# Kernel tuning notes

Measured on AMD Instinct MI355X. Metric: run time of the kernel, lower is better.

## Reference

```python
import jax, jax.numpy as jnp
import numpy as np
from itertools import combinations

NUM_AUG = 10
EPS = 0.01
GAM3 = 0.01
NUM_PAIRS = 500


def setup_inputs() -> dict:
    key = jax.random.key(0)
    m, p = 4000, 256
    kx, ky = jax.random.split(key)
    X = jax.random.normal(kx, (m, p), dtype=jnp.float32)
    y = jax.random.randint(ky, (m,), 0, 400, dtype=jnp.int64)
    num_imgs = m // NUM_AUG
    # deterministic stand-in for np.random.choice over all image pairs
    rng = np.random.default_rng(0)
    pair_combs = np.array(list(combinations(range(num_imgs), 2)))
    sample_idx = rng.choice(len(pair_combs), NUM_PAIRS)
    sample_pairs = jnp.asarray(pair_combs[sample_idx], dtype=jnp.int32)  # [500, 2]
    return {"X": X, "y": y, "sample_pairs": sample_pairs}


def _pair_logdets(X, sample_pairs):
    # X: [m, p] so W = X.T is [p, m]; diagonal Pi selects num_aug columns of W
    # per image, i.e. contiguous rows of X -> W Pi W^T == seg^T @ seg.
    m, p = X.shape
    aug = jnp.arange(NUM_AUG)
    cols_i = sample_pairs[:, 0:1] * NUM_AUG + aug          # [S, 10]
    cols_j = sample_pairs[:, 1:2] * NUM_AUG + aug          # [S, 10]
    cols_pair = jnp.concatenate([cols_i, cols_j], axis=1)  # [S, 20]
    I = jnp.eye(p, dtype=X.dtype)

    def ld(cols, tr_pi):
        seg = X[cols]                                      # [S, k, p]
        gram = jnp.einsum('skp,skq->spq', seg, seg)        # [S, p, p] = W Pi W^T
        scalar = p / ((tr_pi + 1e-8) * EPS)
        return jnp.linalg.slogdet(I + scalar * gram)[1]    # [S]

    ld_pair = ld(cols_pair, 2.0 * NUM_AUG)  # trace(Pi) = 20
    ld_i = ld(cols_i, 1.0 * NUM_AUG)        # trace(Pi_i) = 10
    ld_j = ld(cols_j, 1.0 * NUM_AUG)        # trace(Pi_j) = 10
    return ld_pair, ld_i, ld_j


def reference(X, y, sample_pairs):
    ld_pair, ld_i, ld_j = _pair_logdets(X, sample_pairs)
    compress_loss_empi_ortho = jnp.mean(ld_pair - 0.5 * ld_i - 0.5 * ld_j)
    discrimn_loss_empi = jnp.mean(ld_pair)            # loss_d / num_pairs
    compress_loss_empi = jnp.mean(ld_i + ld_j)        # loss_c / num_pairs (detached in torch)
    total_loss_empi = GAM3 * -compress_loss_empi_ortho
    return (total_loss_empi, discrimn_loss_empi, compress_loss_empi,
            compress_loss_empi_ortho)
```

## Files before the change

kernel.cpp:

```cpp
#include <hip/hip_runtime.h>
#include <math.h>

#define NUM_AUG 10
#define S_PAIRS 500
#define P 256

typedef __attribute__((ext_vector_type(8))) short bf16x8;
typedef __attribute__((ext_vector_type(16))) float f32x16;

#define C_PAIR ((float)(256.0 / ((20.0 + 1e-8) * 0.01)))
#define C_SING ((float)(256.0 / ((10.0 + 1e-8) * 0.01)))

__device__ __forceinline__ unsigned short f2bf(float f) {
  unsigned u = __float_as_uint(f);
  unsigned r = (u + 0x7fffu + ((u >> 16) & 1u)) >> 16;
  return (unsigned short)r;
}

__global__ __launch_bounds__(64) void pair_kernel(
    const float* __restrict__ X,
    const int* __restrict__ pairs,
    float* __restrict__ out2 ) {
  __shared__ uint4 Sb4[32 * 512 / 16];
  __shared__ float G[20][21];
  char* Sb = (char*)Sb4;

  const int s = blockIdx.x;
  const int lane = threadIdx.x;
  const int i0 = pairs[2 * s + 0] * NUM_AUG;
  const int j0 = pairs[2 * s + 1] * NUM_AUG;

#pragma unroll
  for (int r = 0; r < 20; ++r) {
    const int gr = (r < 10) ? (i0 + r) : (j0 + (r - 10));
    const float4 v = *((const float4*)(X + (size_t)gr * P) + lane);
    uint2 w;
    w.x = (unsigned)f2bf(v.x) | ((unsigned)f2bf(v.y) << 16);
    w.y = (unsigned)f2bf(v.z) | ((unsigned)f2bf(v.w) << 16);
    const int off = r * 512 + ((lane * 8) ^ ((r & 15) << 4));
    *(uint2*)(Sb + off) = w;
  }
  __syncthreads();

  const int row = lane & 31;
  const int kg = lane >> 5;
  f32x16 acc0, acc1;
#pragma unroll
  for (int i = 0; i < 16; ++i) { acc0[i] = 0.f; acc1[i] = 0.f; }
#pragma unroll
  for (int kk = 0; kk < 16; ++kk) {
    const int cb = kk * 32 + kg * 16;
    const bf16x8 f = *(const bf16x8*)(Sb + row * 512 + (cb ^ ((row & 15) << 4)));
    if (kk & 1)
      acc1 = __builtin_amdgcn_mfma_f32_32x32x16_bf16(f, f, acc1, 0, 0, 0);
    else
      acc0 = __builtin_amdgcn_mfma_f32_32x32x16_bf16(f, f, acc0, 0, 0, 0);
  }
#pragma unroll
  for (int rg = 0; rg < 16; ++rg) {
    const int grow = (rg & 3) + 8 * (rg >> 2) + 4 * kg;
    if (grow < 20 && row < 20) G[grow][row] = acc0[rg] + acc1[rg];
  }
  __syncthreads();

  const int grp = (lane < 32) ? 0 : (lane < 48) ? 1 : 2;
  const int base = (grp == 0) ? 0 : (grp == 1) ? 32 : 48;
  const int li = lane - base;
  const int n = (grp == 0) ? 20 : 10;
  const float cf = (grp == 0) ? C_PAIR : C_SING;
  const int r0 = (grp == 2) ? 10 : 0;

  float a[20];
#pragma unroll
  for (int k = 0; k < 20; ++k) {
    float g = 0.f;
    if (li < n && k < n) g = G[r0 + li][r0 + k];
    a[k] = cf * g + ((li == k) ? 1.f : 0.f);
  }

  float ld_acc = 0.f;
#pragma unroll
  for (int j = 0; j < 20; ++j) {
    const float dj = __shfl(a[j], base + j, 64);
    const float Ljj = sqrtf(dj);
    const float inv = 1.0f / Ljj;
    const float Lij = a[j] * inv;
    if (li == j && j < n) ld_acc += logf(Ljj);
#pragma unroll
    for (int k = j + 1; k < 20; ++k) {
      const float ck = __shfl(Lij, base + k, 64);
      if (k < n && li >= k) a[k] = fmaf(-Lij, ck, a[k]);
    }
  }

  float vp = (lane < 32) ? ld_acc : 0.f;
  float vs = (lane >= 32) ? ld_acc : 0.f;
#pragma unroll
  for (int m = 1; m < 64; m <<= 1) {
    vp += __shfl_xor(vp, m, 64);
    vs += __shfl_xor(vs, m, 64);
  }
  if (lane == 0) {
    out2[2 * s + 0] = 2.f * vp;
    out2[2 * s + 1] = 2.f * vs;
  }
}

__global__ __launch_bounds__(64) void reduce_kernel(
    const float* __restrict__ out2, float* __restrict__ out) {
  const int lane = threadIdx.x;
  float sp = 0.f, sij = 0.f;
#pragma unroll
  for (int s = lane; s < S_PAIRS; s += 64) {
    const float2 v = *(const float2*)(out2 + 2 * s);
    sp += v.x;
    sij += v.y;
  }
#pragma unroll
  for (int m = 1; m < 64; m <<= 1) {
    sp += __shfl_xor(sp, m, 64);
    sij += __shfl_xor(sij, m, 64);
  }
  if (lane == 0) {
    const float mp = sp / (float)S_PAIRS;
    const float mij = sij / (float)S_PAIRS;
    const float ortho = mp - 0.5f * mij;
    out[0] = -0.01f * ortho;
    out[1] = mp;
    out[2] = mij;
    out[3] = ortho;
  }
}

extern "C" void kernel_launch(void* const* d_in, const int* in_sizes, int n_in,
                              void* d_out, int out_size, void* d_ws, size_t ws_size,
                              hipStream_t stream) {
  const float* X = (const float*)d_in[0];
  const int* pairs = (const int*)d_in[2];
  float* out = (float*)d_out;
  float* ws = (float*)d_ws;

  pair_kernel<<<S_PAIRS, 64, 0, stream>>>(X, pairs, ws);
  reduce_kernel<<<1, 64, 0, stream>>>(ws, out);
}
```

Before: 16.32 us.

## Fuse final reduction into pair kernel via per-block flags and spin-wait

Replaces the separate reduction kernel launch with a last-block reduction inside the pair kernel. Each block publishes its partial sums with a release store and sets a per-block flag, and block S-1 spins until all flags are set, then reduces. A hipMemsetAsync clears the flags before each launch, so the saved kernel launch is swapped for a memset plus a spin-wait. The design can deadlock if block S-1 gets scheduled before other blocks can run, though with 500 small blocks all of them should fit resident on the device.

```diff
diff --git a/kernel.cpp b/kernel.cpp
--- a/kernel.cpp
+++ b/kernel.cpp
@@ -11,16 +11,20 @@
 #define C_PAIR ((float)(256.0 / ((20.0 + 1e-8) * 0.01)))
 #define C_SING ((float)(256.0 / ((10.0 + 1e-8) * 0.01)))
 
+union pack2f { float f[2]; unsigned long long u; };
+
 __device__ __forceinline__ unsigned short f2bf(float f) {
   unsigned u = __float_as_uint(f);
   unsigned r = (u + 0x7fffu + ((u >> 16) & 1u)) >> 16;
   return (unsigned short)r;
 }
 
-__global__ __launch_bounds__(64) void pair_kernel(
+__global__ __launch_bounds__(64) void fused_kernel(
     const float* __restrict__ X,
     const int* __restrict__ pairs,
-    float* __restrict__ out2 ) {
+    unsigned long long* __restrict__ partial,
+    unsigned* __restrict__ flags,
+    float* __restrict__ out) {
   __shared__ uint4 Sb4[32 * 512 / 16];
   __shared__ float G[20][21];
   char* Sb = (char*)Sb4;
@@ -100,35 +104,47 @@
     vp += __shfl_xor(vp, m, 64);
     vs += __shfl_xor(vs, m, 64);
   }
+
   if (lane == 0) {
-    out2[2 * s + 0] = 2.f * vp;
-    out2[2 * s + 1] = 2.f * vs;
+    pack2f p;
+    p.f[0] = 2.f * vp;
+    p.f[1] = 2.f * vs;
+    __hip_atomic_store(&partial[s], p.u, __ATOMIC_RELEASE, __HIP_MEMORY_SCOPE_AGENT);
+    __hip_atomic_store(&flags[s], 1u, __ATOMIC_RELEASE, __HIP_MEMORY_SCOPE_AGENT);
   }
-}
 
-__global__ __launch_bounds__(64) void reduce_kernel(
-    const float* __restrict__ out2, float* __restrict__ out) {
-  const int lane = threadIdx.x;
-  float sp = 0.f, sij = 0.f;
+  if (s == S_PAIRS - 1) {
+    bool mine;
+    do {
+      mine = true;
 #pragma unroll
-  for (int s = lane; s < S_PAIRS; s += 64) {
-    const float2 v = *(const float2*)(out2 + 2 * s);
-    sp += v.x;
-    sij += v.y;
-  }
+      for (int t = lane; t < S_PAIRS; t += 64)
+        mine = mine &&
+               (__hip_atomic_load(&flags[t], __ATOMIC_ACQUIRE, __HIP_MEMORY_SCOPE_AGENT) != 0u);
+    } while (!__all(mine));
+
+    float sp = 0.f, sij = 0.f;
 #pragma unroll
-  for (int m = 1; m < 64; m <<= 1) {
-    sp += __shfl_xor(sp, m, 64);
-    sij += __shfl_xor(sij, m, 64);
-  }
-  if (lane == 0) {
-    const float mp = sp / (float)S_PAIRS;
-    const float mij = sij / (float)S_PAIRS;
-    const float ortho = mp - 0.5f * mij;
-    out[0] = -0.01f * ortho;
-    out[1] = mp;
-    out[2] = mij;
-    out[3] = ortho;
+    for (int t = lane; t < S_PAIRS; t += 64) {
+      pack2f p;
+      p.u = __hip_atomic_load(&partial[t], __ATOMIC_RELAXED, __HIP_MEMORY_SCOPE_AGENT);
+      sp += p.f[0];
+      sij += p.f[1];
+    }
+#pragma unroll
+    for (int m = 1; m < 64; m <<= 1) {
+      sp += __shfl_xor(sp, m, 64);
+      sij += __shfl_xor(sij, m, 64);
+    }
+    if (lane == 0) {
+      const float mp = sp / (float)S_PAIRS;
+      const float mij = sij / (float)S_PAIRS;
+      const float ortho = mp - 0.5f * mij;
+      out[0] = -0.01f * ortho;
+      out[1] = mp;
+      out[2] = mij;
+      out[3] = ortho;
+    }
   }
 }
 
@@ -138,8 +154,10 @@
   const float* X = (const float*)d_in[0];
   const int* pairs = (const int*)d_in[2];
   float* out = (float*)d_out;
-  float* ws = (float*)d_ws;
 
-  pair_kernel<<<S_PAIRS, 64, 0, stream>>>(X, pairs, ws);
-  reduce_kernel<<<1, 64, 0, stream>>>(ws, out);
+  unsigned* flags = (unsigned*)d_ws;
+  unsigned long long* partial = (unsigned long long*)((char*)d_ws + 4096);
+
+  hipMemsetAsync(flags, 0, S_PAIRS * sizeof(unsigned), stream);
+  fused_kernel<<<S_PAIRS, 64, 0, stream>>>(X, pairs, partial, flags, out);
 }
```

Result: slower. 29.58 us (+81.2%).

## Fuse final reduction into pair kernel via packed fixed-point 64-bit atomic

Applied to the files above, without the earlier changes.

Removes the separate reduce kernel. Each block quantizes its two logdet sums to fixed point and packs them, together with a completion counter, into one 64-bit atomic add. The last block to arrive computes the final means. This avoids a second kernel launch but adds a memset launch, and quantization at 1/256 with clamping gives lower precision, with a risk of overflow or negative values wrapping if the inputs change.

```diff
diff --git a/kernel.cpp b/kernel.cpp
--- a/kernel.cpp
+++ b/kernel.cpp
@@ -11,16 +11,21 @@
 #define C_PAIR ((float)(256.0 / ((20.0 + 1e-8) * 0.01)))
 #define C_SING ((float)(256.0 / ((10.0 + 1e-8) * 0.01)))
 
+#define CNT_SHIFT 54
+#define SUM_MASK 0x7FFFFFFull
+#define Q_SCALE 256.f
+
 __device__ __forceinline__ unsigned short f2bf(float f) {
   unsigned u = __float_as_uint(f);
   unsigned r = (u + 0x7fffu + ((u >> 16) & 1u)) >> 16;
   return (unsigned short)r;
 }
 
-__global__ __launch_bounds__(64) void pair_kernel(
+__global__ __launch_bounds__(64) void fused_kernel(
     const float* __restrict__ X,
     const int* __restrict__ pairs,
-    float* __restrict__ out2 ) {
+    unsigned long long* __restrict__ acc,
+    float* __restrict__ out) {
   __shared__ uint4 Sb4[32 * 512 / 16];
   __shared__ float G[20][21];
   char* Sb = (char*)Sb4;
@@ -100,35 +105,28 @@
     vp += __shfl_xor(vp, m, 64);
     vs += __shfl_xor(vs, m, 64);
   }
+
   if (lane == 0) {
-    out2[2 * s + 0] = 2.f * vp;
-    out2[2 * s + 1] = 2.f * vs;
-  }
-}
-
-__global__ __launch_bounds__(64) void reduce_kernel(
-    const float* __restrict__ out2, float* __restrict__ out) {
-  const int lane = threadIdx.x;
-  float sp = 0.f, sij = 0.f;
-#pragma unroll
-  for (int s = lane; s < S_PAIRS; s += 64) {
-    const float2 v = *(const float2*)(out2 + 2 * s);
-    sp += v.x;
-    sij += v.y;
-  }
-#pragma unroll
-  for (int m = 1; m < 64; m <<= 1) {
-    sp += __shfl_xor(sp, m, 64);
-    sij += __shfl_xor(sij, m, 64);
-  }
-  if (lane == 0) {
-    const float mp = sp / (float)S_PAIRS;
-    const float mij = sij / (float)S_PAIRS;
-    const float ortho = mp - 0.5f * mij;
-    out[0] = -0.01f * ortho;
-    out[1] = mp;
-    out[2] = mij;
-    out[3] = ortho;
+    unsigned qp = __float2uint_rn(2.f * vp * Q_SCALE);
+    unsigned qs = __float2uint_rn(2.f * vs * Q_SCALE);
+    qp = (qp > 200000u) ? 200000u : qp;
+    qs = (qs > 200000u) ? 200000u : qs;
+    const unsigned long long add =
+        (1ull << CNT_SHIFT) | ((unsigned long long)qp << 27) | (unsigned long long)qs;
+    const unsigned long long old =
+        __hip_atomic_fetch_add(acc, add, __ATOMIC_RELAXED, __HIP_MEMORY_SCOPE_AGENT);
+    if ((old >> CNT_SHIFT) == (unsigned long long)(S_PAIRS - 1)) {
+      const unsigned long long total = old + add;
+      const float sp = (float)((total >> 27) & SUM_MASK) * (1.f / Q_SCALE);
+      const float sij = (float)(total & SUM_MASK) * (1.f / Q_SCALE);
+      const float mp = sp / (float)S_PAIRS;
+      const float mij = sij / (float)S_PAIRS;
+      const float ortho = mp - 0.5f * mij;
+      out[0] = -0.01f * ortho;
+      out[1] = mp;
+      out[2] = mij;
+      out[3] = ortho;
+    }
   }
 }
 
@@ -138,8 +136,9 @@
   const float* X = (const float*)d_in[0];
   const int* pairs = (const int*)d_in[2];
   float* out = (float*)d_out;
-  float* ws = (float*)d_ws;
 
-  pair_kernel<<<S_PAIRS, 64, 0, stream>>>(X, pairs, ws);
-  reduce_kernel<<<1, 64, 0, stream>>>(ws, out);
+  unsigned long long* acc = (unsigned long long*)d_ws;
+
+  hipMemsetAsync(acc, 0, sizeof(unsigned long long), stream);
+  fused_kernel<<<S_PAIRS, 64, 0, stream>>>(X, pairs, acc, out);
 }
```

Measured after the change: 23.98 us. 46.9% more time.
